# Kernel optimization log

Hardware: AMD Instinct MI355X
Metric: run time of the kernel (lower is better)

Reference implementation:

```python
import jax, jax.numpy as jnp
import numpy as np

BLOCK = 32  # 2**basic_block

def _hadamard(n):
    H = np.array([[1.0]], dtype=np.float32)
    while H.shape[0] < n:
        H = np.block([[H, H], [H, -H]])
    return H


def setup_inputs() -> dict:
    key = jax.random.key(0)
    ks = jax.random.split(key, 9)
    B, T, I, Hd, O = 64, 512, 128, 1024, 128
    sgn = lambda k, shp: jnp.where(jax.random.normal(k, shp) >= 0, 1.0, -1.0).astype(jnp.float32)
    return {
        "x": jax.random.normal(ks[0], (B, T, I), dtype=jnp.float32),
        "W_in": jax.random.normal(ks[1], (I, Hd), dtype=jnp.float32) / np.sqrt(I),
        "s1": sgn(ks[2], (Hd,)),                      # Binadamard sign vector (layer 1)
        "b1": 0.01 * jax.random.normal(ks[3], (Hd,), dtype=jnp.float32),
        "s2": sgn(ks[4], (Hd,)),                      # Binadamard sign vector (layer 2, full)
        "b2": 0.01 * jax.random.normal(ks[5], (Hd,), dtype=jnp.float32),
        "Wbn": sgn(ks[6], (Hd, Hd)) / np.sqrt(Hd),    # BinaryNorm: sign(W)/sqrt(n), materialized
        "W_out": jax.random.normal(ks[7], (Hd, O), dtype=jnp.float32) / np.sqrt(Hd),
        "b_out": jax.random.normal(ks[8], (O,), dtype=jnp.float32),
    }


def reference(x, W_in, s1, b1, s2, b2, Wbn, W_out, b_out):
    B, T, _ = x.shape
    Hd = s1.shape[0]
    Hb = jnp.asarray(_hadamard(BLOCK) / np.sqrt(BLOCK), dtype=x.dtype)   # [32,32]
    Hf = jnp.asarray(_hadamard(Hd) / np.sqrt(Hd), dtype=x.dtype)         # [Hd,Hd]
    u = jnp.einsum('bti,ih->tbh', x, W_in)  # precompute input projections, time-major

    def step(carry, u_t):
        h1, h2 = carry
        # layer 1: block-diagonal sign*Hadamard recurrence + input
        h1 = s1 * (h1.reshape(B, -1, BLOCK) @ Hb).reshape(B, Hd) + b1 + u_t
        h1b = jax.nn.relu(h1)
        # layer 2: full sign*Hadamard recurrence + binary-norm projection of h1b
        h2 = s2 * (h2 @ Hf) + b2 + h1b @ Wbn
        return (h1, h2), None

    h0 = jnp.zeros((B, Hd), dtype=x.dtype)
    (_, h2), _ = jax.lax.scan(step, (h0, h0), u)
    h2b = jax.nn.relu(h2)
    return h2b @ W_out + b_out
```

## Files before the change

### kernel.cpp

```cpp
#include <hip/hip_runtime.h>

#define B_ 64
#define T_ 512
#define I_ 128
#define H_ 1024
#define O_ 128

typedef unsigned short u16;
typedef unsigned int u32;
typedef __attribute__((ext_vector_type(8))) short short8v;
typedef __attribute__((ext_vector_type(4))) float float4v;

typedef __attribute__((address_space(1))) const void gvoid_t;
typedef __attribute__((address_space(3))) void svoid_t;

__device__ __forceinline__ u16 f2bf(float f) {
  union { float f; u32 u; } v; v.f = f;
  u32 r = v.u + 0x7FFF + ((v.u >> 16) & 1);
  return (u16)(r >> 16);
}
__device__ __forceinline__ float bf2f(u16 b) {
  union { u32 u; float f; } v; v.u = ((u32)b) << 16;
  return v.f;
}
__device__ __forceinline__ float bits2f(u32 b) {
  union { u32 u; float f; } v; v.u = b;
  return v.f;
}

__device__ __forceinline__ float fwht32(float x, int lane) {
#pragma unroll
  for (int s = 1; s <= 16; s <<= 1) {
    const float y = __shfl_xor(x, s);
    x = (lane & s) ? (y - x) : (x + y);
  }
  return x;
}

__device__ __forceinline__ void fwht32_reg(float* x) {
#pragma unroll
  for (int s = 1; s < 32; s <<= 1)
#pragma unroll
    for (int i = 0; i < 32; ++i)
      if (!(i & s)) { const float a = x[i], b = x[i | s]; x[i] = a + b; x[i | s] = a - b; }
}

__device__ __forceinline__ void transpose32(float* x, float (*T)[33], int t) {
#pragma unroll
  for (int c = 0; c < 32; ++c) T[t][c] = x[c];
#pragma unroll
  for (int c = 0; c < 32; ++c) x[c] = T[c][t];
}

__global__ __launch_bounds__(256) void prep_all(const float* __restrict__ x, const float* __restrict__ Wbn,
                                                const float* __restrict__ W_in, u16* __restrict__ xT,
                                                u16* __restrict__ WbnT, u16* __restrict__ WinT) {
  const int blk = blockIdx.x;
  if (blk < 4096) {
    const int idx = blk * 256 + threadIdx.x;
    const int n = idx >> 10, k = idx & 1023;
    WbnT[idx] = f2bf(Wbn[(size_t)k * 1024 + n]);
  } else if (blk < 4608) {
    const int idx = (blk - 4096) * 256 + threadIdx.x;
    const int n = idx >> 7, k = idx & 127;
    WinT[idx] = f2bf(W_in[(size_t)k * 1024 + n]);
  } else {
    const int idx = (blk - 4608) * 256 + threadIdx.x;
    const int i = idx & (I_ - 1);
    const int r = idx >> 7;
    const int b = r & (B_ - 1);
    const int t = r >> 6;
    xT[idx] = f2bf(x[((size_t)b * T_ + t) * I_ + i]);
  }
}

template <int K, bool BIAS>
__global__ __launch_bounds__(256) void gemm_bf16(const u16* __restrict__ A, const u16* __restrict__ Bt,
                                                 u16* __restrict__ C, const float* __restrict__ bias) {
  __shared__ u16 As[128 * 64];
  __shared__ u16 Bs[128 * 64];
  const int tid = threadIdx.x;
  const int bm = blockIdx.x, bn = blockIdx.y;
  const int lane = tid & 63, w = tid >> 6;
  const int wr = w >> 1, wc = w & 1;
  const int l16 = lane & 15, lq = lane >> 4;

  float4v acc[4][4];
#pragma unroll
  for (int mi = 0; mi < 4; ++mi)
#pragma unroll
    for (int ni = 0; ni < 4; ++ni)
#pragma unroll
      for (int j = 0; j < 4; ++j) acc[mi][ni][j] = 0.f;

  const int srow = w * 32 + (lane >> 3);
  const int scol = (((lane & 7) ^ (lane >> 3)) << 3);
  const u16* Ag = A + (size_t)(bm * 128 + srow) * K + scol;
  const u16* Bg = Bt + (size_t)(bn * 128 + srow) * K + scol;

  for (int k0 = 0; k0 < K; k0 += 64) {
    __syncthreads();
#pragma unroll
    for (int i = 0; i < 4; ++i) {
      __builtin_amdgcn_global_load_lds((gvoid_t*)(Ag + k0 + (size_t)i * 8 * K),
                                       (svoid_t*)&As[(w * 32 + i * 8) * 64], 16, 0, 0);
      __builtin_amdgcn_global_load_lds((gvoid_t*)(Bg + k0 + (size_t)i * 8 * K),
                                       (svoid_t*)&Bs[(w * 32 + i * 8) * 64], 16, 0, 0);
    }
    __syncthreads();
#pragma unroll
    for (int ks = 0; ks < 2; ++ks) {
      short8v a[4], bf[4];
#pragma unroll
      for (int mi = 0; mi < 4; ++mi) {
        const int row = wr * 64 + mi * 16 + l16;
        a[mi] = *(const short8v*)&As[row * 64 + (((ks * 4 + lq) ^ (row & 7)) << 3)];
      }
#pragma unroll
      for (int ni = 0; ni < 4; ++ni) {
        const int row = wc * 64 + ni * 16 + l16;
        bf[ni] = *(const short8v*)&Bs[row * 64 + (((ks * 4 + lq) ^ (row & 7)) << 3)];
      }
#pragma unroll
      for (int mi = 0; mi < 4; ++mi)
#pragma unroll
        for (int ni = 0; ni < 4; ++ni)
          acc[mi][ni] = __builtin_amdgcn_mfma_f32_16x16x32_bf16(a[mi], bf[ni], acc[mi][ni], 0, 0, 0);
    }
  }

#pragma unroll
  for (int mi = 0; mi < 4; ++mi)
#pragma unroll
    for (int ni = 0; ni < 4; ++ni) {
      const int row = bm * 128 + wr * 64 + mi * 16 + lq * 4;
      const int col = bn * 128 + wc * 64 + ni * 16 + l16;
      const float bv = BIAS ? bias[col] : 0.f;
#pragma unroll
      for (int j = 0; j < 4; ++j) C[(size_t)(row + j) * H_ + col] = f2bf(acc[mi][ni][j] + bv);
    }
}

__global__ __launch_bounds__(1024) void h1_Pinit(const float* __restrict__ s1, float* __restrict__ P) {
  const int hb = blockIdx.x;
  const int tid = threadIdx.x;
  const int j = tid >> 5, r = tid & 31;
  const int lane = tid & 63;
  const float sc = s1[hb * 32 + r] * 0.17677669529663687f;
  float x = (r == j) ? 1.f : 0.f;
  for (int it = 0; it < 16; ++it) x = sc * fwht32(x, lane);
  P[(size_t)hb * 1024 + r * 32 + j] = x;
}

__global__ __launch_bounds__(64) void h1_local(const u16* __restrict__ u, const float* __restrict__ s1,
                                               float* __restrict__ Ybuf) {
  const int g = blockIdx.x * 64 + threadIdx.x;
  const int hb = g & 31, b = (g >> 5) & 63, chunk = g >> 11;
  float x[32], sc[32];
#pragma unroll
  for (int i = 0; i < 32; i += 4) {
    const float4 s4 = *(const float4*)&s1[hb * 32 + i];
    sc[i] = s4.x * 0.17677669529663687f;
    sc[i + 1] = s4.y * 0.17677669529663687f;
    sc[i + 2] = s4.z * 0.17677669529663687f;
    sc[i + 3] = s4.w * 0.17677669529663687f;
  }
#pragma unroll
  for (int i = 0; i < 32; ++i) x[i] = 0.f;
  const u16* up = u + ((size_t)(chunk * 16) * B_ + b) * H_ + hb * 32;
#pragma unroll 2
  for (int k = 0; k < 16; ++k) {
    u32 wv[16];
#pragma unroll
    for (int j = 0; j < 4; ++j) {
      const uint4 t4 = *(const uint4*)(up + (size_t)k * (B_ * H_) + j * 8);
      wv[4 * j] = t4.x; wv[4 * j + 1] = t4.y; wv[4 * j + 2] = t4.z; wv[4 * j + 3] = t4.w;
    }
    fwht32_reg(x);
#pragma unroll
    for (int i2 = 0; i2 < 16; ++i2) {
      x[2 * i2]     = fmaf(sc[2 * i2],     x[2 * i2],     bits2f(wv[i2] << 16));
      x[2 * i2 + 1] = fmaf(sc[2 * i2 + 1], x[2 * i2 + 1], bits2f(wv[i2] & 0xFFFF0000u));
    }
  }
  float* yp = Ybuf + (size_t)g * 32;
#pragma unroll
  for (int i = 0; i < 32; i += 4) {
    float4 o; o.x = x[i]; o.y = x[i + 1]; o.z = x[i + 2]; o.w = x[i + 3];
    *(float4*)(yp + i) = o;
  }
}

__global__ __launch_bounds__(64) void h1_carry(const float* __restrict__ P, const float* __restrict__ Ybuf,
                                               float* __restrict__ Zbuf) {
  const int hpair = blockIdx.x, b = blockIdx.y;
  const int lane = threadIdx.x;
  const int r = lane & 31, hb = hpair * 2 + (lane >> 5);
  const float* Prow = P + (size_t)hb * 1024 + r * 32;
  float pr[32];
#pragma unroll
  for (int j = 0; j < 32; ++j) pr[j] = Prow[j];
  float z = 0.f;
  const int base = lane & 32;
  for (int c = 0; c < 32; ++c) {
    Zbuf[(((size_t)c * 64 + b) * 32 + hb) * 32 + r] = z;
    if (c < 31) {
      const float yv = Ybuf[(((size_t)c * 64 + b) * 32 + hb) * 32 + r];
      float zn = 0.f;
#pragma unroll
      for (int j = 0; j < 32; ++j) zn = fmaf(pr[j], __shfl(z, base + j), zn);
      z = zn + yv;
    }
  }
}

__global__ __launch_bounds__(64) void h1_apply(u16* __restrict__ u, const float* __restrict__ s1,
                                               const float* __restrict__ Zbuf) {
  const int g = blockIdx.x * 64 + threadIdx.x;
  const int hb = g & 31, b = (g >> 5) & 63, chunk = g >> 11;
  float x[32], sc[32];
#pragma unroll
  for (int i = 0; i < 32; i += 4) {
    const float4 s4 = *(const float4*)&s1[hb * 32 + i];
    sc[i] = s4.x * 0.17677669529663687f;
    sc[i + 1] = s4.y * 0.17677669529663687f;
    sc[i + 2] = s4.z * 0.17677669529663687f;
    sc[i + 3] = s4.w * 0.17677669529663687f;
  }
  const float* zp = Zbuf + (size_t)g * 32;
#pragma unroll
  for (int i = 0; i < 32; i += 4) {
    const float4 z4 = *(const float4*)(zp + i);
    x[i] = z4.x; x[i + 1] = z4.y; x[i + 2] = z4.z; x[i + 3] = z4.w;
  }
  u16* up = u + ((size_t)(chunk * 16) * B_ + b) * H_ + hb * 32;
#pragma unroll 2
  for (int k = 0; k < 16; ++k) {
    u32 wv[16];
#pragma unroll
    for (int j = 0; j < 4; ++j) {
      const uint4 t4 = *(const uint4*)(up + (size_t)k * (B_ * H_) + j * 8);
      wv[4 * j] = t4.x; wv[4 * j + 1] = t4.y; wv[4 * j + 2] = t4.z; wv[4 * j + 3] = t4.w;
    }
    fwht32_reg(x);
#pragma unroll
    for (int i2 = 0; i2 < 16; ++i2) {
      x[2 * i2]     = fmaf(sc[2 * i2],     x[2 * i2],     bits2f(wv[i2] << 16));
      x[2 * i2 + 1] = fmaf(sc[2 * i2 + 1], x[2 * i2 + 1], bits2f(wv[i2] & 0xFFFF0000u));
    }
    u32 ov[16];
#pragma unroll
    for (int i2 = 0; i2 < 16; ++i2) {
      const u32 lo = f2bf(fmaxf(x[2 * i2], 0.f));
      const u32 hi = f2bf(fmaxf(x[2 * i2 + 1], 0.f));
      ov[i2] = lo | (hi << 16);
    }
#pragma unroll
    for (int j = 0; j < 4; ++j) {
      uint4 t4; t4.x = ov[4 * j]; t4.y = ov[4 * j + 1]; t4.z = ov[4 * j + 2]; t4.w = ov[4 * j + 3];
      *(uint4*)(up + (size_t)k * (B_ * H_) + j * 8) = t4;
    }
  }
}

__global__ __launch_bounds__(256) void fwht_chunk(const u16* __restrict__ V, const float* __restrict__ s2,
                                                  u16* __restrict__ A32, u16* __restrict__ Y) {
  __shared__ float tr[4][2][32][33];
  const int wv = threadIdx.x >> 6;
  const int lane = threadIdx.x & 63;
  const int slot = lane >> 5, t = lane & 31;
  float (*T)[33] = tr[wv][slot];
  const int gs = blockIdx.x * 8 + wv * 2 + slot;

  float x[32], s0[32], s1[32];
#pragma unroll
  for (int c = 0; c < 32; ++c) {
    s0[c] = s2[t * 32 + c] * 0.03125f;
    s1[c] = s2[c * 32 + t] * 0.03125f;
  }

  if (gs < 1024) {
    const int W = gs;
#pragma unroll
    for (int c = 0; c < 32; ++c) x[c] = (t * 32 + c == W) ? 1.f : 0.f;
    for (int j = 0; j < 32; ++j) {
      if (j & 1) {
#pragma unroll
        for (int c = 0; c < 32; ++c) x[c] *= s1[c];
      } else {
#pragma unroll
        for (int c = 0; c < 32; ++c) x[c] *= s0[c];
      }
      fwht32_reg(x);
      transpose32(x, T, t);
      fwht32_reg(x);
    }
    u16* dst = A32 + (size_t)W * H_ + t * 32;
    u32 ov[16];
#pragma unroll
    for (int c = 0; c < 16; ++c) ov[c] = (u32)f2bf(x[2 * c]) | ((u32)f2bf(x[2 * c + 1]) << 16);
#pragma unroll
    for (int j = 0; j < 4; ++j) {
      uint4 t4; t4.x = ov[4 * j]; t4.y = ov[4 * j + 1]; t4.z = ov[4 * j + 2]; t4.w = ov[4 * j + 3];
      *(uint4*)(dst + j * 8) = t4;
    }
  } else {
    const int s = gs - 1024;
    const int c0 = s >> 6, b = s & 63;
    const u16* Vbase = V + ((size_t)(c0 * 32) * B_ + b) * H_;
#pragma unroll
    for (int c = 0; c < 32; ++c) x[c] = 0.f;
    for (int j = 0; j < 32; ++j) {
      const u16* vrow = Vbase + (size_t)j * (B_ * H_);
      const int pe = (j + 1) & 1;
      u32 vpk[16];
      u16 vsc[32];
      if (pe == 0) {
#pragma unroll
        for (int q = 0; q < 4; ++q) {
          const uint4 t4 = *(const uint4*)(vrow + t * 32 + q * 8);
          vpk[4 * q] = t4.x; vpk[4 * q + 1] = t4.y; vpk[4 * q + 2] = t4.z; vpk[4 * q + 3] = t4.w;
        }
      } else {
#pragma unroll
        for (int c = 0; c < 32; ++c) vsc[c] = vrow[c * 32 + t];
      }
      fwht32_reg(x);
      transpose32(x, T, t);
      fwht32_reg(x);
      if (pe == 0) {
#pragma unroll
        for (int c = 0; c < 16; ++c) {
          x[2 * c]     = fmaf(s0[2 * c],     x[2 * c],     bits2f(vpk[c] << 16));
          x[2 * c + 1] = fmaf(s0[2 * c + 1], x[2 * c + 1], bits2f(vpk[c] & 0xFFFF0000u));
        }
      } else {
#pragma unroll
        for (int c = 0; c < 32; ++c) x[c] = fmaf(s1[c], x[c], bf2f(vsc[c]));
      }
    }
    u16* dst = Y + ((size_t)c0 * B_ + b) * H_ + t * 32;
    u32 ov[16];
#pragma unroll
    for (int c = 0; c < 16; ++c) ov[c] = (u32)f2bf(x[2 * c]) | ((u32)f2bf(x[2 * c + 1]) << 16);
#pragma unroll
    for (int j = 0; j < 4; ++j) {
      uint4 t4; t4.x = ov[4 * j]; t4.y = ov[4 * j + 1]; t4.z = ov[4 * j + 2]; t4.w = ov[4 * j + 3];
      *(uint4*)(dst + j * 8) = t4;
    }
  }
}

template <bool FIRST, bool LAST>
__global__ __launch_bounds__(256) void combine(const u16* __restrict__ Zold, const u16* __restrict__ Yc,
                                               const u16* __restrict__ A32, u16* __restrict__ Znew,
                                               float* __restrict__ h2out) {
  const int rt = blockIdx.x >> 6, nt = blockIdx.x & 63;
  const int tid = threadIdx.x;
  __shared__ float red[4][16][16];
  if (!FIRST) {
    const int w = tid >> 6, lane = tid & 63, l16 = lane & 15, lq = lane >> 4;
    float4v acc = {0.f, 0.f, 0.f, 0.f};
    const u16* Ap = Zold + (size_t)(rt * 16 + l16) * H_ + w * 256 + lq * 8;
    const u16* Bp = A32 + (size_t)(nt * 16 + l16) * H_ + w * 256 + lq * 8;
#pragma unroll
    for (int ks = 0; ks < 8; ++ks) {
      short8v a = *(const short8v*)(Ap + ks * 32);
      short8v bb = *(const short8v*)(Bp + ks * 32);
      acc = __builtin_amdgcn_mfma_f32_16x16x32_bf16(a, bb, acc, 0, 0, 0);
    }
#pragma unroll
    for (int j = 0; j < 4; ++j) red[w][lq * 4 + j][l16] = acc[j];
    __syncthreads();
  } else {
    __syncthreads();
  }
  const int row = tid >> 4, col = tid & 15;
  float s = 0.f;
  if (!FIRST) s = red[0][row][col] + red[1][row][col] + red[2][row][col] + red[3][row][col];
  const int b = rt * 16 + row, n = nt * 16 + col;
  s += bf2f(Yc[(size_t)b * H_ + n]);
  if (LAST) h2out[(size_t)b * H_ + n] = s;
  else Znew[(size_t)b * H_ + n] = f2bf(s);
}

__global__ __launch_bounds__(128) void final_out(const float* __restrict__ h2, const float* __restrict__ W_out,
                                                 const float* __restrict__ b_out, float* __restrict__ out) {
  __shared__ float hrow[H_];
  const int b = blockIdx.x, o = threadIdx.x;
  for (int i = o; i < H_; i += 128) hrow[i] = fmaxf(h2[(size_t)b * H_ + i], 0.f);
  __syncthreads();
  float acc = b_out[o];
  for (int h = 0; h < H_; ++h) acc = fmaf(hrow[h], W_out[(size_t)h * O_ + o], acc);
  out[b * O_ + o] = acc;
}

extern "C" void kernel_launch(void* const* d_in, const int* in_sizes, int n_in,
                              void* d_out, int out_size, void* d_ws, size_t ws_size,
                              hipStream_t stream) {
  const float* x     = (const float*)d_in[0];
  const float* W_in  = (const float*)d_in[1];
  const float* s1    = (const float*)d_in[2];
  const float* b1    = (const float*)d_in[3];
  const float* s2    = (const float*)d_in[4];
  const float* b2    = (const float*)d_in[5];
  const float* Wbn   = (const float*)d_in[6];
  const float* W_out = (const float*)d_in[7];
  const float* b_out = (const float*)d_in[8];
  float* out = (float*)d_out;

  char* ws = (char*)d_ws;
  u16* u      = (u16*)ws;
  u16* V      = (u16*)(ws + 67108864);
  float* P1   = (float*)(ws + 67108864);
  float* Zbuf = (float*)(ws + 69206016);
  u16* xT     = (u16*)(ws + 134217728);
  float* Ybuf = (float*)(ws + 134217728);
  u16* WbnT   = (u16*)(ws + 142606336);
  u16* WinT   = (u16*)(ws + 144703488);
  u16* A32    = (u16*)(ws + 134217728);
  u16* Y      = (u16*)(ws + 136314880);
  u16* Zb0    = (u16*)(ws + 138412032);
  u16* Zb1    = (u16*)(ws + 138543104);
  float* h2   = (float*)(ws + 138674176);

  prep_all<<<20992, 256, 0, stream>>>(x, Wbn, W_in, xT, WbnT, WinT);
  h1_Pinit<<<32, 1024, 0, stream>>>(s1, P1);
  gemm_bf16<128, true><<<dim3(256, 8), 256, 0, stream>>>(xT, WinT, u, b1);
  h1_local<<<1024, 64, 0, stream>>>(u, s1, Ybuf);
  h1_carry<<<dim3(16, 64), 64, 0, stream>>>(P1, Ybuf, Zbuf);
  h1_apply<<<1024, 64, 0, stream>>>(u, s1, Zbuf);
  gemm_bf16<1024, true><<<dim3(256, 8), 256, 0, stream>>>(u, WbnT, V, b2);
  fwht_chunk<<<256, 256, 0, stream>>>(V, s2, A32, Y);

  u16* Zb[2] = {Zb0, Zb1};
  combine<true, false><<<256, 256, 0, stream>>>(nullptr, Y, A32, Zb[0], nullptr);
  for (int c = 1; c < 15; ++c)
    combine<false, false><<<256, 256, 0, stream>>>(Zb[(c + 1) & 1], Y + (size_t)c * B_ * H_, A32,
                                                   Zb[c & 1], nullptr);
  combine<false, true><<<256, 256, 0, stream>>>(Zb[0], Y + (size_t)15 * B_ * H_, A32, nullptr, h2);

  final_out<<<64, 128, 0, stream>>>(h2, W_out, b_out, out);
}
```

Before: 327.8 us.

## Fuse pairs of chunk-combine steps using precomputed A^64 and A^32 matrices

The fwht_chunk kernel now computes the transition matrix for 64 steps as well as for 32 steps and stores both side by side in a widened Bt2 buffer. The sequential combine chain then advances two chunks per launch by multiplying [Zold | Ymid] against [A64; A32] with a doubled K dimension. This cuts the number of serial combine launches from 16 to 8, reducing launch and latency overhead on the critical path. In exchange, the matrix-generation work doubles, each combine does twice the MFMA work, and there is one extra bf16 rounding of the higher matrix power.

```diff
diff --git a/kernel.cpp b/kernel.cpp
--- a/kernel.cpp
+++ b/kernel.cpp
@@ -264,7 +264,7 @@
 }
 
 __global__ __launch_bounds__(256) void fwht_chunk(const u16* __restrict__ V, const float* __restrict__ s2,
-                                                  u16* __restrict__ A32, u16* __restrict__ Y) {
+                                                  u16* __restrict__ Bt2, u16* __restrict__ Y) {
   __shared__ float tr[4][2][32][33];
   const int wv = threadIdx.x >> 6;
   const int lane = threadIdx.x & 63;
@@ -283,7 +283,7 @@
     const int W = gs;
 #pragma unroll
     for (int c = 0; c < 32; ++c) x[c] = (t * 32 + c == W) ? 1.f : 0.f;
-    for (int j = 0; j < 32; ++j) {
+    for (int j = 0; j < 64; ++j) {
       if (j & 1) {
 #pragma unroll
         for (int c = 0; c < 32; ++c) x[c] *= s1[c];
@@ -294,15 +294,26 @@
       fwht32_reg(x);
       transpose32(x, T, t);
       fwht32_reg(x);
-    }
-    u16* dst = A32 + (size_t)W * H_ + t * 32;
+      if (j == 31) {
+        u16* dst = Bt2 + (size_t)W * 2048 + 1024 + t * 32;
+        u32 ov[16];
+#pragma unroll
+        for (int c = 0; c < 16; ++c) ov[c] = (u32)f2bf(x[2 * c]) | ((u32)f2bf(x[2 * c + 1]) << 16);
+#pragma unroll
+        for (int q = 0; q < 4; ++q) {
+          uint4 t4; t4.x = ov[4 * q]; t4.y = ov[4 * q + 1]; t4.z = ov[4 * q + 2]; t4.w = ov[4 * q + 3];
+          *(uint4*)(dst + q * 8) = t4;
+        }
+      }
+    }
+    u16* dst = Bt2 + (size_t)W * 2048 + t * 32;
     u32 ov[16];
 #pragma unroll
     for (int c = 0; c < 16; ++c) ov[c] = (u32)f2bf(x[2 * c]) | ((u32)f2bf(x[2 * c + 1]) << 16);
 #pragma unroll
-    for (int j = 0; j < 4; ++j) {
-      uint4 t4; t4.x = ov[4 * j]; t4.y = ov[4 * j + 1]; t4.z = ov[4 * j + 2]; t4.w = ov[4 * j + 3];
-      *(uint4*)(dst + j * 8) = t4;
+    for (int q = 0; q < 4; ++q) {
+      uint4 t4; t4.x = ov[4 * q]; t4.y = ov[4 * q + 1]; t4.z = ov[4 * q + 2]; t4.w = ov[4 * q + 3];
+      *(uint4*)(dst + q * 8) = t4;
     }
   } else {
     const int s = gs - 1024;
@@ -351,35 +362,43 @@
   }
 }
 
-template <bool FIRST, bool LAST>
-__global__ __launch_bounds__(256) void combine(const u16* __restrict__ Zold, const u16* __restrict__ Yc,
-                                               const u16* __restrict__ A32, u16* __restrict__ Znew,
-                                               float* __restrict__ h2out) {
+template <bool DOUBLE, bool LAST>
+__global__ __launch_bounds__(256) void combine2(const u16* __restrict__ Zold, const u16* __restrict__ Ymid,
+                                                const u16* __restrict__ Yadd, const u16* __restrict__ Bt2,
+                                                u16* __restrict__ Znew, float* __restrict__ h2out) {
   const int rt = blockIdx.x >> 6, nt = blockIdx.x & 63;
   const int tid = threadIdx.x;
   __shared__ float red[4][16][16];
-  if (!FIRST) {
-    const int w = tid >> 6, lane = tid & 63, l16 = lane & 15, lq = lane >> 4;
-    float4v acc = {0.f, 0.f, 0.f, 0.f};
+  const int w = tid >> 6, lane = tid & 63, l16 = lane & 15, lq = lane >> 4;
+  float4v acc = {0.f, 0.f, 0.f, 0.f};
+  if (DOUBLE) {
+    const u16* Arow = (w < 2) ? (Zold + (size_t)(rt * 16 + l16) * H_ + w * 512)
+                              : (Ymid + (size_t)(rt * 16 + l16) * H_ + (w - 2) * 512);
+    const u16* Ap = Arow + lq * 8;
+    const u16* Bp = Bt2 + (size_t)(nt * 16 + l16) * 2048 + w * 512 + lq * 8;
+#pragma unroll
+    for (int ks = 0; ks < 16; ++ks) {
+      short8v a = *(const short8v*)(Ap + ks * 32);
+      short8v bb = *(const short8v*)(Bp + ks * 32);
+      acc = __builtin_amdgcn_mfma_f32_16x16x32_bf16(a, bb, acc, 0, 0, 0);
+    }
+  } else {
     const u16* Ap = Zold + (size_t)(rt * 16 + l16) * H_ + w * 256 + lq * 8;
-    const u16* Bp = A32 + (size_t)(nt * 16 + l16) * H_ + w * 256 + lq * 8;
+    const u16* Bp = Bt2 + (size_t)(nt * 16 + l16) * 2048 + 1024 + w * 256 + lq * 8;
 #pragma unroll
     for (int ks = 0; ks < 8; ++ks) {
       short8v a = *(const short8v*)(Ap + ks * 32);
       short8v bb = *(const short8v*)(Bp + ks * 32);
       acc = __builtin_amdgcn_mfma_f32_16x16x32_bf16(a, bb, acc, 0, 0, 0);
     }
-#pragma unroll
-    for (int j = 0; j < 4; ++j) red[w][lq * 4 + j][l16] = acc[j];
-    __syncthreads();
-  } else {
-    __syncthreads();
-  }
+  }
+#pragma unroll
+  for (int j = 0; j < 4; ++j) red[w][lq * 4 + j][l16] = acc[j];
+  __syncthreads();
   const int row = tid >> 4, col = tid & 15;
-  float s = 0.f;
-  if (!FIRST) s = red[0][row][col] + red[1][row][col] + red[2][row][col] + red[3][row][col];
+  float s = red[0][row][col] + red[1][row][col] + red[2][row][col] + red[3][row][col];
   const int b = rt * 16 + row, n = nt * 16 + col;
-  s += bf2f(Yc[(size_t)b * H_ + n]);
+  s += bf2f(Yadd[(size_t)b * H_ + n]);
   if (LAST) h2out[(size_t)b * H_ + n] = s;
   else Znew[(size_t)b * H_ + n] = f2bf(s);
 }
@@ -418,11 +437,11 @@
   float* Ybuf = (float*)(ws + 134217728);
   u16* WbnT   = (u16*)(ws + 142606336);
   u16* WinT   = (u16*)(ws + 144703488);
-  u16* A32    = (u16*)(ws + 134217728);
-  u16* Y      = (u16*)(ws + 136314880);
-  u16* Zb0    = (u16*)(ws + 138412032);
-  u16* Zb1    = (u16*)(ws + 138543104);
-  float* h2   = (float*)(ws + 138674176);
+  u16* Bt2    = (u16*)(ws + 134217728);
+  u16* Y      = (u16*)(ws + 138412032);
+  u16* Zb0    = (u16*)(ws + 140509184);
+  u16* Zb1    = (u16*)(ws + 140640256);
+  float* h2   = (float*)(ws + 140771328);
 
   prep_all<<<20992, 256, 0, stream>>>(x, Wbn, W_in, xT, WbnT, WinT);
   h1_Pinit<<<32, 1024, 0, stream>>>(s1, P1);
@@ -431,14 +450,17 @@
   h1_carry<<<dim3(16, 64), 64, 0, stream>>>(P1, Ybuf, Zbuf);
   h1_apply<<<1024, 64, 0, stream>>>(u, s1, Zbuf);
   gemm_bf16<1024, true><<<dim3(256, 8), 256, 0, stream>>>(u, WbnT, V, b2);
-  fwht_chunk<<<256, 256, 0, stream>>>(V, s2, A32, Y);
-
-  u16* Zb[2] = {Zb0, Zb1};
-  combine<true, false><<<256, 256, 0, stream>>>(nullptr, Y, A32, Zb[0], nullptr);
-  for (int c = 1; c < 15; ++c)
-    combine<false, false><<<256, 256, 0, stream>>>(Zb[(c + 1) & 1], Y + (size_t)c * B_ * H_, A32,
-                                                   Zb[c & 1], nullptr);
-  combine<false, true><<<256, 256, 0, stream>>>(Zb[0], Y + (size_t)15 * B_ * H_, A32, nullptr, h2);
+  fwht_chunk<<<256, 256, 0, stream>>>(V, s2, Bt2, Y);
+
+  const size_t BH = (size_t)B_ * H_;
+  combine2<true, false><<<256, 256, 0, stream>>>(Y,            Y + 1 * BH,  Y + 2 * BH,  Bt2, Zb0, nullptr);
+  combine2<true, false><<<256, 256, 0, stream>>>(Zb0,          Y + 3 * BH,  Y + 4 * BH,  Bt2, Zb1, nullptr);
+  combine2<true, false><<<256, 256, 0, stream>>>(Zb1,          Y + 5 * BH,  Y + 6 * BH,  Bt2, Zb0, nullptr);
+  combine2<true, false><<<256, 256, 0, stream>>>(Zb0,          Y + 7 * BH,  Y + 8 * BH,  Bt2, Zb1, nullptr);
+  combine2<true, false><<<256, 256, 0, stream>>>(Zb1,          Y + 9 * BH,  Y + 10 * BH, Bt2, Zb0, nullptr);
+  combine2<true, false><<<256, 256, 0, stream>>>(Zb0,          Y + 11 * BH, Y + 12 * BH, Bt2, Zb1, nullptr);
+  combine2<true, false><<<256, 256, 0, stream>>>(Zb1,          Y + 13 * BH, Y + 14 * BH, Bt2, Zb0, nullptr);
+  combine2<false, true><<<256, 256, 0, stream>>>(Zb0,          nullptr,     Y + 15 * BH, Bt2, nullptr, h2);
 
   final_out<<<64, 128, 0, stream>>>(h2, W_out, b_out, out);
 }
```

Measured after the change: 331.1 us. No clear change (+1.0%).
